# Kernel optimization log

Measured on AMD Instinct MI355X. Metric: run time of the kernel, lower is better.

## Reference

```python
import jax, jax.numpy as jnp
import numpy as np

# Config mirroring TransFusionHead / HungarianAssigner3D defaults (nuScenes)
PC_RANGE = (-54.0, -54.0, -5.0, 54.0, 54.0, 3.0)
CLS_W, CLS_ALPHA, CLS_GAMMA = 0.15, 0.25, 2.0
REG_W, IOU_W = 0.25, 0.25
EPS = 1e-12

B, N, M, C = 8, 4096, 1024, 10


def setup_inputs() -> dict:
    key = jax.random.key(0)
    k1, k2, k3, k4 = jax.random.split(key, 4)

    def make_boxes(k, n):
        ka, kb, kc, kd = jax.random.split(k, 4)
        xy = jax.random.uniform(ka, (B, n, 2), minval=-54.0, maxval=54.0)
        z = jax.random.uniform(kb, (B, n, 1), minval=-5.0, maxval=3.0)
        dims = jax.random.uniform(kc, (B, n, 3), minval=0.5, maxval=6.0)
        yaw = jax.random.uniform(kd, (B, n, 1), minval=-np.pi, maxval=np.pi)
        return jnp.concatenate([xy, z, dims, yaw], axis=-1).astype(jnp.float32)

    bboxes = make_boxes(k1, N)          # [B, N, 7]
    gt_bboxes = make_boxes(k2, M)       # [B, M, 7]
    cls_pred = jax.random.normal(k3, (B, N, C), dtype=jnp.float32)  # logits
    gt_labels = jax.random.randint(k4, (B, M), 0, C).astype(jnp.int32)
    return {"bboxes": bboxes, "gt_bboxes": gt_bboxes,
            "cls_pred": cls_pred, "gt_labels": gt_labels}


def _bev_iou(a, b):
    # a: [B,N,7], b: [B,M,7] -> axis-aligned BEV IoU [B,N,M]
    xa1 = a[..., 0] - a[..., 3] * 0.5; ya1 = a[..., 1] - a[..., 4] * 0.5
    xa2 = a[..., 0] + a[..., 3] * 0.5; ya2 = a[..., 1] + a[..., 4] * 0.5
    xb1 = b[..., 0] - b[..., 3] * 0.5; yb1 = b[..., 1] - b[..., 4] * 0.5
    xb2 = b[..., 0] + b[..., 3] * 0.5; yb2 = b[..., 1] + b[..., 4] * 0.5
    ix1 = jnp.maximum(xa1[:, :, None], xb1[:, None, :])
    iy1 = jnp.maximum(ya1[:, :, None], yb1[:, None, :])
    ix2 = jnp.minimum(xa2[:, :, None], xb2[:, None, :])
    iy2 = jnp.minimum(ya2[:, :, None], yb2[:, None, :])
    inter = jnp.clip(ix2 - ix1, 0) * jnp.clip(iy2 - iy1, 0)
    area_a = jnp.clip(xa2 - xa1, 0) * jnp.clip(ya2 - ya1, 0)
    area_b = jnp.clip(xb2 - xb1, 0) * jnp.clip(yb2 - yb1, 0)
    union = area_a[:, :, None] + area_b[:, None, :] - inter
    return inter / jnp.clip(union, 1e-6)


def reference(bboxes, gt_bboxes, cls_pred, gt_labels):
    # --- focal classification cost ---
    p = jax.nn.sigmoid(cls_pred)                                   # [B,N,C]
    neg = -jnp.log(1.0 - p + EPS) * (1.0 - CLS_ALPHA) * p ** CLS_GAMMA
    pos = -jnp.log(p + EPS) * CLS_ALPHA * (1.0 - p) ** CLS_GAMMA
    diff = (pos - neg) * CLS_W                                     # [B,N,C]
    idx = jnp.broadcast_to(gt_labels[:, None, :], (diff.shape[0], diff.shape[1], gt_labels.shape[1]))
    cls_cost = jnp.take_along_axis(diff, idx, axis=2)              # [B,N,M]

    pc_start = jnp.asarray(PC_RANGE[0:2], dtype=bboxes.dtype)
    pc_rng = jnp.asarray(PC_RANGE[3:5], dtype=bboxes.dtype) - pc_start
    a_xy = (bboxes[..., :2] - pc_start) / pc_rng                   # [B,N,2]
    b_xy = (gt_bboxes[..., :2] - pc_start) / pc_rng                # [B,M,2]
    reg_cost = jnp.abs(a_xy[:, :, None, :] - b_xy[:, None, :, :]).sum(-1) * REG_W

    # --- IoU cost (axis-aligned BEV IoU, CPU path of lidar_box_iou3d) ---
    iou = _bev_iou(bboxes, gt_bboxes)                              # [B,N,M]

    cost = cls_cost + reg_cost - iou * IOU_W
    return cost
```

## Files before the change

kernel.cpp:

```cpp
#include <hip/hip_runtime.h>
#include <hip/hip_bf16.h>

#define BB 8
#define NN 4096
#define MM 1024
#define CC 10

#define ROWS_PER_WAVE 8
#define ROWS_PER_BLOCK 32
#define BLOCKS_PER_BATCH (NN / ROWS_PER_BLOCK)

__global__ __launch_bounds__(256, 2)
void transfusion_cost_kernel(const float* __restrict__ bboxes,
                             const float* __restrict__ gt_bboxes,
                             const float* __restrict__ cls_pred,
                             const int*   __restrict__ gt_labels,
                             float* __restrict__ out)
{
    const int tid  = threadIdx.x;
    const int lane = tid & 63;
    const int wave = tid >> 6;

    const int bk = blockIdx.x;
    const int b  = bk / BLOCKS_PER_BATCH;
    const int n0 = (bk % BLOCKS_PER_BATCH) * ROWS_PER_BLOCK + wave * ROWS_PER_WAVE;

    const float* gtb = gt_bboxes + (size_t)b * MM * 7;
    const int*   gtl = gt_labels + (size_t)b * MM;

    const float SCL = 0.25f / 108.0f;

    float gx1[16], gy1[16], gx2[16], gy2[16];
    float areaB[16], bxs[16], bys[16];
    int   lbl[16];

#pragma unroll
    for (int i = 0; i < 16; ++i) {
        const int m = lane + 64 * i;
        const float* g = gtb + m * 7;
        const float x  = g[0];
        const float y  = g[1];
        const float dx = g[3];
        const float dy = g[4];
        const float x1 = x - 0.5f * dx, x2 = x + 0.5f * dx;
        const float y1 = y - 0.5f * dy, y2 = y + 0.5f * dy;
        gx1[i] = x1; gy1[i] = y1; gx2[i] = x2; gy2[i] = y2;
        areaB[i] = fmaxf(x2 - x1, 0.0f) * fmaxf(y2 - y1, 0.0f);
        bxs[i] = (x + 54.0f) * SCL;
        bys[i] = (y + 54.0f) * SCL;
        lbl[i] = gtl[m];
    }

    for (int r = 0; r < ROWS_PER_WAVE; ++r) {
        const int n = n0 + r;

        const float* a = bboxes + ((size_t)b * NN + n) * 7;
        const float ax  = a[0];
        const float ay  = a[1];
        const float adx = a[3];
        const float ady = a[4];
        const float xa1 = ax - 0.5f * adx, xa2 = ax + 0.5f * adx;
        const float ya1 = ay - 0.5f * ady, ya2 = ay + 0.5f * ady;
        const float areaA = fmaxf(xa2 - xa1, 0.0f) * fmaxf(ya2 - ya1, 0.0f);
        const float axs = (ax + 54.0f) * SCL;
        const float ays = (ay + 54.0f) * SCL;

        const int c = (lane < CC) ? lane : 0;
        const float logit = cls_pred[((size_t)b * NN + n) * CC + c];
        const float p   = 1.0f / (1.0f + expf(-logit));
        const float omp = 1.0f - p;
        const float pos = -logf(p   + 1e-12f) * 0.25f * omp * omp;
        const float neg = -logf(omp + 1e-12f) * 0.75f * p * p;
        const float dval = (pos - neg) * 0.15f;

        float* orow = out + ((size_t)b * NN + n) * MM;

#pragma unroll
        for (int i = 0; i < 16; ++i) {
            const int m = lane + 64 * i;

            const float ix1 = fmaxf(xa1, gx1[i]);
            const float iy1 = fmaxf(ya1, gy1[i]);
            const float ix2 = fminf(xa2, gx2[i]);
            const float iy2 = fminf(ya2, gy2[i]);
            const float iw  = fmaxf(ix2 - ix1, 0.0f);
            const float ih  = fmaxf(iy2 - iy1, 0.0f);
            const float inter = iw * ih;
            const float uni   = areaA + areaB[i] - inter;
            const float iou   = inter / fmaxf(uni, 1e-6f);

            const float cls = __shfl(dval, lbl[i], 64);
            const float reg = fabsf(axs - bxs[i]) + fabsf(ays - bys[i]);

            orow[m] = cls + reg - 0.25f * iou;
        }
    }
}

extern "C" void kernel_launch(void* const* d_in, const int* in_sizes, int n_in,
                              void* d_out, int out_size, void* d_ws, size_t ws_size,
                              hipStream_t stream) {
    const float* bboxes    = (const float*)d_in[0];
    const float* gt_bboxes = (const float*)d_in[1];
    const float* cls_pred  = (const float*)d_in[2];
    const int*   gt_labels = (const int*)d_in[3];
    float* out = (float*)d_out;

    const int grid = BB * BLOCKS_PER_BATCH;
    transfusion_cost_kernel<<<grid, 256, 0, stream>>>(bboxes, gt_bboxes, cls_pred,
                                                      gt_labels, out);
}
```

Before: 167.8 us.

## Split GT columns across waves with float4 stores and fast reciprocal

Work is redistributed so each wave owns 256 GT columns (4 contiguous per lane) and loops over all 32 block rows, in place of each wave owning 8 rows across all 1024 columns. Per-lane GT register state drops from 16 to 4 entries, so launch bounds rise to 4 blocks per CU, and output is written as float4 vector stores. The IoU division becomes a hardware v_rcp_f32, which is slightly less accurate. Each wave now recomputes the focal classification value for 32 rows instead of 8.

```diff
diff --git a/kernel.cpp b/kernel.cpp
--- a/kernel.cpp
+++ b/kernel.cpp
@@ -6,11 +6,16 @@
 #define MM 1024
 #define CC 10
 
-#define ROWS_PER_WAVE 8
 #define ROWS_PER_BLOCK 32
 #define BLOCKS_PER_BATCH (NN / ROWS_PER_BLOCK)
 
-__global__ __launch_bounds__(256, 2)
+__device__ __forceinline__ float fast_rcp(float x) {
+    float r;
+    asm("v_rcp_f32 %0, %1" : "=v"(r) : "v"(x));
+    return r;
+}
+
+__global__ __launch_bounds__(256, 4)
 void transfusion_cost_kernel(const float* __restrict__ bboxes,
                              const float* __restrict__ gt_bboxes,
                              const float* __restrict__ cls_pred,
@@ -21,79 +26,80 @@
     const int lane = tid & 63;
     const int wave = tid >> 6;
 
-    const int bk = blockIdx.x;
-    const int b  = bk / BLOCKS_PER_BATCH;
-    const int n0 = (bk % BLOCKS_PER_BATCH) * ROWS_PER_BLOCK + wave * ROWS_PER_WAVE;
-
-    const float* gtb = gt_bboxes + (size_t)b * MM * 7;
-    const int*   gtl = gt_labels + (size_t)b * MM;
+    const int b  = blockIdx.x / BLOCKS_PER_BATCH;
+    const int n0 = (blockIdx.x % BLOCKS_PER_BATCH) * ROWS_PER_BLOCK;
 
     const float SCL = 0.25f / 108.0f;
 
-    float gx1[16], gy1[16], gx2[16], gy2[16];
-    float areaB[16], bxs[16], bys[16];
-    int   lbl[16];
+    const int m0 = wave * 256 + 4 * lane;
+    const float* gtb = gt_bboxes + ((size_t)b * MM + m0) * 7;
+    const int*   gtl = gt_labels + (size_t)b * MM + m0;
 
+    float gx1[4], gy1[4], gx2[4], gy2[4], areaB[4], bxs[4], bys[4];
+    int   lbl[4];
 #pragma unroll
-    for (int i = 0; i < 16; ++i) {
-        const int m = lane + 64 * i;
-        const float* g = gtb + m * 7;
+    for (int j = 0; j < 4; ++j) {
+        const float* g = gtb + j * 7;
         const float x  = g[0];
         const float y  = g[1];
         const float dx = g[3];
         const float dy = g[4];
         const float x1 = x - 0.5f * dx, x2 = x + 0.5f * dx;
         const float y1 = y - 0.5f * dy, y2 = y + 0.5f * dy;
-        gx1[i] = x1; gy1[i] = y1; gx2[i] = x2; gy2[i] = y2;
-        areaB[i] = fmaxf(x2 - x1, 0.0f) * fmaxf(y2 - y1, 0.0f);
-        bxs[i] = (x + 54.0f) * SCL;
-        bys[i] = (y + 54.0f) * SCL;
-        lbl[i] = gtl[m];
+        gx1[j] = x1; gy1[j] = y1; gx2[j] = x2; gy2[j] = y2;
+        areaB[j] = fmaxf(x2 - x1, 0.0f) * fmaxf(y2 - y1, 0.0f);
+        bxs[j] = (x + 54.0f) * SCL;
+        bys[j] = (y + 54.0f) * SCL;
+        lbl[j] = gtl[j];
     }
 
-    for (int r = 0; r < ROWS_PER_WAVE; ++r) {
-        const int n = n0 + r;
+    const int c = (lane < CC) ? lane : 0;
+    const float* arow = bboxes   + ((size_t)b * NN + n0) * 7;
+    const float* crow = cls_pred + ((size_t)b * NN + n0) * CC;
+    float*       orow = out + ((size_t)b * NN + n0) * MM + m0;
 
-        const float* a = bboxes + ((size_t)b * NN + n) * 7;
+#pragma unroll 2
+    for (int r = 0; r < ROWS_PER_BLOCK; ++r) {
+        const float* a = arow + r * 7;
         const float ax  = a[0];
         const float ay  = a[1];
         const float adx = a[3];
         const float ady = a[4];
+        const float logit = crow[r * CC + c];
+
         const float xa1 = ax - 0.5f * adx, xa2 = ax + 0.5f * adx;
         const float ya1 = ay - 0.5f * ady, ya2 = ay + 0.5f * ady;
         const float areaA = fmaxf(xa2 - xa1, 0.0f) * fmaxf(ya2 - ya1, 0.0f);
         const float axs = (ax + 54.0f) * SCL;
         const float ays = (ay + 54.0f) * SCL;
 
-        const int c = (lane < CC) ? lane : 0;
-        const float logit = cls_pred[((size_t)b * NN + n) * CC + c];
         const float p   = 1.0f / (1.0f + expf(-logit));
         const float omp = 1.0f - p;
         const float pos = -logf(p   + 1e-12f) * 0.25f * omp * omp;
         const float neg = -logf(omp + 1e-12f) * 0.75f * p * p;
         const float dval = (pos - neg) * 0.15f;
 
-        float* orow = out + ((size_t)b * NN + n) * MM;
-
+        float vv[4];
 #pragma unroll
-        for (int i = 0; i < 16; ++i) {
-            const int m = lane + 64 * i;
-
-            const float ix1 = fmaxf(xa1, gx1[i]);
-            const float iy1 = fmaxf(ya1, gy1[i]);
-            const float ix2 = fminf(xa2, gx2[i]);
-            const float iy2 = fminf(ya2, gy2[i]);
+        for (int j = 0; j < 4; ++j) {
+            const float ix1 = fmaxf(xa1, gx1[j]);
+            const float iy1 = fmaxf(ya1, gy1[j]);
+            const float ix2 = fminf(xa2, gx2[j]);
+            const float iy2 = fminf(ya2, gy2[j]);
             const float iw  = fmaxf(ix2 - ix1, 0.0f);
             const float ih  = fmaxf(iy2 - iy1, 0.0f);
             const float inter = iw * ih;
-            const float uni   = areaA + areaB[i] - inter;
-            const float iou   = inter / fmaxf(uni, 1e-6f);
+            const float uni   = areaA + areaB[j] - inter;
+            const float iou   = inter * fast_rcp(fmaxf(uni, 1e-6f));
 
-            const float cls = __shfl(dval, lbl[i], 64);
-            const float reg = fabsf(axs - bxs[i]) + fabsf(ays - bys[i]);
+            const float cls = __shfl(dval, lbl[j], 64);
+            const float reg = fabsf(axs - bxs[j]) + fabsf(ays - bys[j]);
 
-            orow[m] = cls + reg - 0.25f * iou;
+            vv[j] = cls + reg - 0.25f * iou;
         }
+
+        *reinterpret_cast<float4*>(orow + (size_t)r * MM) =
+            make_float4(vv[0], vv[1], vv[2], vv[3]);
     }
 }
 
```

New measurement: 170.3 us. No clear change (+1.5%).
